# Optimization experiments

Measured on AMD Instinct MI355X. Metric: run time of the kernel, lower is better.

The kernel has to match this reference:

```python
import jax, jax.numpy as jnp
import numpy as np

N_HEAD = 16

def setup_inputs() -> dict:
    key = jax.random.key(0)
    k1, k2, k3 = jax.random.split(key, 3)
    B, T, D = 2, 2048, 1024
    x = jax.random.normal(k1, (B, T, D), dtype=jnp.float32)
    sigma_qkv = float(np.sqrt(2.0 / (D + 3 * D)))
    sigma_out = float(np.sqrt(2.0 / (D + D)))
    W_qkv = jax.random.truncated_normal(k2, -3.0, 3.0, (3 * D, D), dtype=jnp.float32) * sigma_qkv
    W_out = jax.random.truncated_normal(k3, -3.0, 3.0, (D, D), dtype=jnp.float32) * sigma_out
    return {"x": x, "W_qkv": W_qkv, "W_out": W_out}


def reference(x, W_qkv, W_out):
    B, T, C = x.shape
    H = N_HEAD
    hd = C // H
    qkv = x @ W_qkv.T  # (B,T,3C)
    q, k, v = jnp.split(qkv, 3, axis=-1)
    # (B,T,C) -> (B,H,T,hd)
    q = q.reshape(B, T, H, hd).transpose(0, 2, 1, 3)
    k = k.reshape(B, T, H, hd).transpose(0, 2, 1, 3)
    v = v.reshape(B, T, H, hd).transpose(0, 2, 1, 3)
    scale = 1.0 / jnp.sqrt(jnp.asarray(hd, dtype=x.dtype))
    score = jnp.einsum('bhqd,bhkd->bhqk', q, k) * scale  # (B,H,T,T)
    causal = jnp.tril(jnp.ones((T, T), dtype=bool))
    score = jnp.where(causal, score, -jnp.inf)
    attn = jax.nn.softmax(score, axis=-1)
    out = jnp.einsum('bhqk,bhkd->bhqd', attn, v)  # (B,H,T,hd)
    out = out.transpose(0, 2, 1, 3).reshape(B, T, C)
    return out @ W_out.T
```

## Files before the change

### kernel.cpp

```cpp
#include <hip/hip_runtime.h>
#include <hip/hip_bf16.h>
#include <cstdint>

typedef unsigned short u16;
typedef __attribute__((ext_vector_type(8))) short bf16x8;
typedef __attribute__((ext_vector_type(4))) float f32x4;

#define T_SEQ 2048
#define NHEAD 16
#define HDIM  64
#define NB    2

__device__ __forceinline__ float bf2f(uint32_t h) { return __uint_as_float(h << 16); }
__device__ __forceinline__ u16 f2bf(float f) {
    uint32_t u = __float_as_uint(f);
    u += 0x7fffu + ((u >> 16) & 1u);
    return (u16)(u >> 16);
}

__device__ __forceinline__ void gl_lds16(const u16* g, u16* s) {
    __builtin_amdgcn_global_load_lds(
        (const __attribute__((address_space(1))) unsigned int*)g,
        (__attribute__((address_space(3))) unsigned int*)s, 16, 0, 0);
}

__global__ void detect_dtype(const uint32_t* __restrict__ x, int* __restrict__ flag) {
    __shared__ int red[4];
    int c = 0;
#pragma unroll
    for (int j = 0; j < 4; j++) {
        uint32_t v = x[threadIdx.x * 4 + j];
        uint32_t lo = v & 0xffffu;
        uint32_t e = (lo >> 7) & 0xffu;
        if (lo != 0u && e >= 110u && e <= 135u) c++;
    }
#pragma unroll
    for (int off = 32; off; off >>= 1) c += __shfl_down(c, off);
    if ((threadIdx.x & 63) == 0) red[threadIdx.x >> 6] = c;
    __syncthreads();
    if (threadIdx.x == 0)
        *flag = (red[0] + red[1] + red[2] + red[3] > 614) ? 1 : 0;
}

__global__ __launch_bounds__(256) void to_bf16(
    const void* __restrict__ src, u16* __restrict__ dst, int n4,
    const int* __restrict__ flag)
{
    int i = blockIdx.x * 256 + threadIdx.x;
    const int stride = gridDim.x * 256;
    if (*flag != 0) {
        const uint2* s = (const uint2*)src;
        uint2* d = (uint2*)dst;
        for (; i < n4; i += stride) d[i] = s[i];
    } else {
        const float4* s = (const float4*)src;
        for (; i < n4; i += stride) {
            float4 v = s[i];
            ushort4 o = { f2bf(v.x), f2bf(v.y), f2bf(v.z), f2bf(v.w) };
            *(ushort4*)(dst + (size_t)i * 4) = o;
        }
    }
}

template<int BM, int MODE>
__global__ __launch_bounds__(256, 3) void gemm_bt_mfma(
    const u16* __restrict__ A, const u16* __restrict__ B,
    int N, int K,
    u16* __restrict__ qo, u16* __restrict__ ko, u16* __restrict__ vt,
    u16* __restrict__ outb16, float* __restrict__ outf32,
    const int* __restrict__ flag)
{
    constexpr int WM = BM / 2;
    constexpr int MI = WM / 16;
    constexpr int IA = BM / 32;
    constexpr int ST = 2 * BM * 64 * 2;
    constexpr int E16 = 4 * WM * 72 * 2;
    constexpr int EF = (MODE == 1) ? 4 * WM * (WM + 4) * 4 : 0;
    constexpr int SB = (ST > E16 ? ST : E16) > EF ? (ST > E16 ? ST : E16) : EF;
    __shared__ u16 smem[SB / 2];
    u16* As = smem;
    u16* Bs = smem + BM * 64;
    const int tid = threadIdx.x;
    const int bm = blockIdx.y * BM, bn = blockIdx.x * BM;
    const int w = tid >> 6, lane = tid & 63;
    const int wm = (w >> 1) * WM, wn = (w & 1) * WM;
    const int n16 = lane & 15, quad = lane >> 4;
    const int l8 = lane >> 3, c8 = lane & 7;

    f32x4 acc[MI][MI];
#pragma unroll
    for (int mi = 0; mi < MI; mi++)
#pragma unroll
        for (int ni = 0; ni < MI; ni++) acc[mi][ni] = (f32x4){0.f, 0.f, 0.f, 0.f};

    const int KT = K >> 6;
    for (int kt = 0; kt < KT; kt++) {
        const int k0 = kt << 6;
#pragma unroll
        for (int i = 0; i < IA; i++) {
            int rowblk = (i * 4 + w) * 8;
            int row = rowblk + l8;
            int gcol = (c8 ^ l8) * 8;
            gl_lds16(A + (size_t)(bm + row) * K + k0 + gcol, As + rowblk * 64);
            gl_lds16(B + (size_t)(bn + row) * K + k0 + gcol, Bs + rowblk * 64);
        }
        __syncthreads();
#pragma unroll
        for (int ks = 0; ks < 2; ks++) {
            bf16x8 af[MI], bfr[MI];
#pragma unroll
            for (int mi = 0; mi < MI; mi++) {
                int row = wm + mi * 16 + n16;
                af[mi] = *(const bf16x8*)(As + row * 64 + (((ks * 4 + quad) ^ (n16 & 7)) * 8));
            }
#pragma unroll
            for (int ni = 0; ni < MI; ni++) {
                int row = wn + ni * 16 + n16;
                bfr[ni] = *(const bf16x8*)(Bs + row * 64 + (((ks * 4 + quad) ^ (n16 & 7)) * 8));
            }
#pragma unroll
            for (int mi = 0; mi < MI; mi++)
#pragma unroll
                for (int ni = 0; ni < MI; ni++)
                    acc[mi][ni] = __builtin_amdgcn_mfma_f32_16x16x32_bf16(
                        af[mi], bfr[ni], acc[mi][ni], 0, 0, 0);
        }
        __syncthreads();
    }

    if constexpr (MODE == 0) {
        u16* ep = smem + w * (WM * 72);
        const int which = (bn + wn) >> 10;
        const int hq = ((bn + wn) & 1023) >> 6;
        const int bb = (bm + wm) >> 11;
        const int tb = (bm + wm) & (T_SEQ - 1);
        if (which == 2) {
#pragma unroll
            for (int mi = 0; mi < MI; mi++)
#pragma unroll
                for (int ni = 0; ni < MI; ni++)
#pragma unroll
                    for (int r = 0; r < 4; r++)
                        ep[(ni * 16 + n16) * 72 + mi * 16 + quad * 4 + r] = f2bf(acc[mi][ni][r]);
            asm volatile("s_waitcnt lgkmcnt(0)" ::: "memory");
            u16* dst = vt + ((size_t)(bb * NHEAD + hq) * HDIM) * T_SEQ + tb;
#pragma unroll
            for (int it = 0; it < 8; it++) {
                int row = it * 8 + l8, col = c8 * 8;
                bf16x8 v = *(const bf16x8*)(ep + row * 72 + col);
                *(bf16x8*)(dst + (size_t)row * T_SEQ + col) = v;
            }
        } else {
            const float sc = which ? 1.f : 0.125f;
#pragma unroll
            for (int mi = 0; mi < MI; mi++)
#pragma unroll
                for (int ni = 0; ni < MI; ni++)
#pragma unroll
                    for (int r = 0; r < 4; r++)
                        ep[(mi * 16 + quad * 4 + r) * 72 + ni * 16 + n16] = f2bf(acc[mi][ni][r] * sc);
            asm volatile("s_waitcnt lgkmcnt(0)" ::: "memory");
            u16* dst = (which ? ko : qo) + ((size_t)(bb * NHEAD + hq) * T_SEQ + tb) * HDIM;
#pragma unroll
            for (int it = 0; it < 8; it++) {
                int row = it * 8 + l8, col = c8 * 8;
                bf16x8 v = *(const bf16x8*)(ep + row * 72 + col);
                *(bf16x8*)(dst + (size_t)row * HDIM + col) = v;
            }
        }
    } else {
        if (*flag == 0) {
            float* epf = (float*)smem + w * (WM * (WM + 4));
#pragma unroll
            for (int mi = 0; mi < MI; mi++)
#pragma unroll
                for (int ni = 0; ni < MI; ni++)
#pragma unroll
                    for (int r = 0; r < 4; r++)
                        epf[(mi * 16 + quad * 4 + r) * (WM + 4) + ni * 16 + n16] = acc[mi][ni][r];
            asm volatile("s_waitcnt lgkmcnt(0)" ::: "memory");
            constexpr int LPR = WM / 4;
            constexpr int RPI = 64 / LPR;
#pragma unroll
            for (int it = 0; it < WM / RPI; it++) {
                int row = it * RPI + lane / LPR, col = (lane % LPR) * 4;
                float4 v = *(const float4*)(epf + row * (WM + 4) + col);
                *(float4*)(outf32 + (size_t)(bm + wm + row) * N + bn + wn + col) = v;
            }
        } else {
            u16* ep = smem + w * (WM * 72);
#pragma unroll
            for (int mi = 0; mi < MI; mi++)
#pragma unroll
                for (int ni = 0; ni < MI; ni++)
#pragma unroll
                    for (int r = 0; r < 4; r++)
                        ep[(mi * 16 + quad * 4 + r) * 72 + ni * 16 + n16] = f2bf(acc[mi][ni][r]);
            asm volatile("s_waitcnt lgkmcnt(0)" ::: "memory");
            constexpr int LPR = WM / 8;
            constexpr int RPI = 64 / LPR;
#pragma unroll
            for (int it = 0; it < WM / RPI; it++) {
                int row = it * RPI + lane / LPR, col = (lane % LPR) * 8;
                bf16x8 v = *(const bf16x8*)(ep + row * 72 + col);
                *(bf16x8*)(outb16 + (size_t)(bm + wm + row) * N + bn + wn + col) = v;
            }
        }
    }
}

__global__ __launch_bounds__(512, 4) void attn_mfma(
    const u16* __restrict__ qb, const u16* __restrict__ kb,
    const u16* __restrict__ vt, u16* __restrict__ ob)
{
    __shared__ u16 Ks[64 * 64];
    __shared__ u16 Vs[64 * 64];
    __shared__ u16 Plds[8][16][72];
    const int bidx = blockIdx.x;
    const int c = bidx & 255;
    const int rr = bidx >> 8;
    const int bh = c & 31;
    const int jm = c >> 5;
    const int t = rr ? (15 - jm) : jm;
    const int w = threadIdx.x >> 6, lane = threadIdx.x & 63;
    const int n16 = lane & 15, quad = lane >> 4;
    const int l8 = lane >> 3, c8 = lane & 7;
    const size_t baseK = (size_t)bh * T_SEQ * HDIM;
    const size_t baseV = (size_t)bh * HDIM * T_SEQ;
    const int b = bh >> 4, head = bh & 15;

    bf16x8 ones;
#pragma unroll
    for (int e = 0; e < 8; e++) ones[e] = (short)0x3F80;

    auto stage = [&](int kt) {
        int row = w * 8 + l8;
        int gc = (c8 ^ l8) * 8;
        gl_lds16(kb + baseK + (size_t)(kt * 64 + row) * HDIM + gc, Ks + (w * 8) * 64);
        gl_lds16(vt + baseV + (size_t)row * T_SEQ + (size_t)kt * 64 + gc, Vs + (w * 8) * 64);
    };

    const int qrow = t * 128 + w * 16;
    bf16x8 qf[2];
#pragma unroll
    for (int ks = 0; ks < 2; ks++)
        qf[ks] = *(const bf16x8*)(qb + baseK + (size_t)(qrow + n16) * HDIM + ks * 32 + quad * 8);

    f32x4 accO[4];
#pragma unroll
    for (int st = 0; st < 4; st++) accO[st] = (f32x4){0.f, 0.f, 0.f, 0.f};
    f32x4 accL = (f32x4){0.f, 0.f, 0.f, 0.f};

    const int ktmax = 2 * t + 1;
    const int kend  = 2 * t + (w >> 2);

    stage(0);
    for (int kt = 0; kt <= ktmax; kt++) {
        __syncthreads();

        const bool act = (kt <= kend);
        bf16x8 kf[2][4], vf[2][4];
        if (act) {
#pragma unroll
            for (int st = 0; st < 4; st++)
#pragma unroll
                for (int ks = 0; ks < 2; ks++) {
                    int off = (st * 16 + n16) * 64 + (((ks * 4 + quad) ^ (n16 & 7)) * 8);
                    kf[ks][st] = *(const bf16x8*)(Ks + off);
                    vf[ks][st] = *(const bf16x8*)(Vs + off);
                }
        }
        __syncthreads();

        if (kt < ktmax) stage(kt + 1);

        if (act) {
            f32x4 S[4];
#pragma unroll
            for (int st = 0; st < 4; st++) S[st] = (f32x4){0.f, 0.f, 0.f, 0.f};
#pragma unroll
            for (int st = 0; st < 4; st++)
#pragma unroll
                for (int ks = 0; ks < 2; ks++)
                    S[st] = __builtin_amdgcn_mfma_f32_16x16x32_bf16(qf[ks], kf[ks][st], S[st], 0, 0, 0);
            if (kt == kend) {
                int qloc = (w & 3) * 16 + quad * 4;
#pragma unroll
                for (int st = 0; st < 4; st++) {
                    int kloc = st * 16 + n16;
#pragma unroll
                    for (int r = 0; r < 4; r++)
                        if (kloc > qloc + r) S[st][r] = -INFINITY;
                }
            }
#pragma unroll
            for (int st = 0; st < 4; st++)
#pragma unroll
                for (int r = 0; r < 4; r++) {
                    float pv = exp2f(__builtin_fmaf(S[st][r], 1.44269504f, -14.4269504f));
                    Plds[w][quad * 4 + r][st * 16 + n16] = (u16)(__float_as_uint(pv) >> 16);
                }
            asm volatile("s_waitcnt lgkmcnt(0)" ::: "memory");
            bf16x8 pf[2];
#pragma unroll
            for (int ks = 0; ks < 2; ks++)
                pf[ks] = *(const bf16x8*)(&Plds[w][n16][ks * 32 + quad * 8]);
#pragma unroll
            for (int st = 0; st < 4; st++)
#pragma unroll
                for (int ks = 0; ks < 2; ks++)
                    accO[st] = __builtin_amdgcn_mfma_f32_16x16x32_bf16(pf[ks], vf[ks][st], accO[st], 0, 0, 0);
#pragma unroll
            for (int ks = 0; ks < 2; ks++)
                accL = __builtin_amdgcn_mfma_f32_16x16x32_bf16(pf[ks], ones, accL, 0, 0, 0);
        }
    }

#pragma unroll
    for (int r = 0; r < 4; r++) {
        float inv = 1.f / accL[r];
#pragma unroll
        for (int st = 0; st < 4; st++)
            Plds[w][quad * 4 + r][st * 16 + n16] = f2bf(accO[st][r] * inv);
    }
    asm volatile("s_waitcnt lgkmcnt(0)" ::: "memory");
    u16* dst = ob + ((size_t)(b * T_SEQ + qrow)) * 1024 + head * HDIM;
#pragma unroll
    for (int it = 0; it < 2; it++) {
        int row = it * 8 + l8, col = c8 * 8;
        bf16x8 v = *(const bf16x8*)(&Plds[w][row][col]);
        *(bf16x8*)(dst + (size_t)row * 1024 + col) = v;
    }
}

extern "C" void kernel_launch(void* const* d_in, const int* in_sizes, int n_in,
                              void* d_out, int out_size, void* d_ws, size_t ws_size,
                              hipStream_t stream) {
    const void* x    = d_in[0];
    const void* Wqkv = d_in[1];
    const void* Wout = d_in[2];

    const int Mtok = NB * T_SEQ;
    const size_t n_x    = (size_t)Mtok * 1024;
    const size_t n_wqkv = (size_t)3072 * 1024;
    const size_t n_wout = (size_t)1024 * 1024;
    const size_t qkv_elems = (size_t)NB * NHEAD * T_SEQ * HDIM;

    u16* xb    = (u16*)d_ws;
    u16* wqkvb = xb + n_x;
    u16* woutb = wqkvb + n_wqkv;
    u16* qb    = woutb + n_wout;
    u16* kb    = qb + qkv_elems;
    u16* vt    = kb + qkv_elems;
    u16* obuf  = vt + qkv_elems;
    int* flag  = (int*)(obuf + qkv_elems);

    detect_dtype<<<1, 256, 0, stream>>>((const uint32_t*)x, flag);

    to_bf16<<<1024, 256, 0, stream>>>(x,    xb,    (int)(n_x / 4),    flag);
    to_bf16<<<1024, 256, 0, stream>>>(Wqkv, wqkvb, (int)(n_wqkv / 4), flag);
    to_bf16<<<512,  256, 0, stream>>>(Wout, woutb, (int)(n_wout / 4), flag);

    gemm_bt_mfma<128, 0><<<dim3(3072 / 128, Mtok / 128), 256, 0, stream>>>(
        xb, wqkvb, 3072, 1024, qb, kb, vt, nullptr, nullptr, flag);

    attn_mfma<<<dim3(NB * NHEAD * (T_SEQ / 128)), 512, 0, stream>>>(qb, kb, vt, obuf);

    gemm_bt_mfma<64, 1><<<dim3(1024 / 64, Mtok / 64), 256, 0, stream>>>(
        obuf, woutb, 1024, 1024, nullptr, nullptr, nullptr,
        (u16*)d_out, (float*)d_out, flag);
}
```

Baseline: 171.1 us.

## Split attention KV loop across two warp groups with LDS combine

Doubles the attention block to 1024 threads. Two groups of 8 warps each handle alternating 64-key tiles for the same 128 query rows, then combine partial outputs and row sums through shared memory before normalising. Block scheduling also changes to longest-first ordering, replacing the previous paired balancing. This halves the serial KV-loop length per block, in exchange for an extra combine step, larger blocks and more register and LDS pressure per CU. The softmax uses a fixed max offset, so partial sums add directly.

After: 177.6 us. 1.04x slower.

```diff
diff --git a/kernel.cpp b/kernel.cpp
--- a/kernel.cpp
+++ b/kernel.cpp
@@ -209,38 +209,40 @@
     }
 }
 
-__global__ __launch_bounds__(512, 4) void attn_mfma(
+__global__ __launch_bounds__(1024, 4) void attn_mfma(
     const u16* __restrict__ qb, const u16* __restrict__ kb,
     const u16* __restrict__ vt, u16* __restrict__ ob)
 {
-    __shared__ u16 Ks[64 * 64];
-    __shared__ u16 Vs[64 * 64];
-    __shared__ u16 Plds[8][16][72];
+    __shared__ u16 KV[4 * 64 * 64];
+    __shared__ u16 Plds[16][16][72];
     const int bidx = blockIdx.x;
-    const int c = bidx & 255;
-    const int rr = bidx >> 8;
-    const int bh = c & 31;
-    const int jm = c >> 5;
-    const int t = rr ? (15 - jm) : jm;
+    const int bh = bidx & 31;
+    const int t  = 15 - (bidx >> 5);
     const int w = threadIdx.x >> 6, lane = threadIdx.x & 63;
+    const int g = w >> 3;
+    const int wq = w & 7;
     const int n16 = lane & 15, quad = lane >> 4;
     const int l8 = lane >> 3, c8 = lane & 7;
     const size_t baseK = (size_t)bh * T_SEQ * HDIM;
     const size_t baseV = (size_t)bh * HDIM * T_SEQ;
     const int b = bh >> 4, head = bh & 15;
 
+    u16* Ksg = KV + g * (2 * 64 * 64);
+    u16* Vsg = KV + g * (2 * 64 * 64) + 64 * 64;
+
     bf16x8 ones;
 #pragma unroll
     for (int e = 0; e < 8; e++) ones[e] = (short)0x3F80;
 
-    auto stage = [&](int kt) {
-        int row = w * 8 + l8;
+    auto stage = [&](int i) {
+        int kt = 2 * i + g;
+        int row = wq * 8 + l8;
         int gc = (c8 ^ l8) * 8;
-        gl_lds16(kb + baseK + (size_t)(kt * 64 + row) * HDIM + gc, Ks + (w * 8) * 64);
-        gl_lds16(vt + baseV + (size_t)row * T_SEQ + (size_t)kt * 64 + gc, Vs + (w * 8) * 64);
+        gl_lds16(kb + baseK + (size_t)(kt * 64 + row) * HDIM + gc, Ksg + (wq * 8) * 64);
+        gl_lds16(vt + baseV + (size_t)row * T_SEQ + (size_t)kt * 64 + gc, Vsg + (wq * 8) * 64);
     };
 
-    const int qrow = t * 128 + w * 16;
+    const int qrow = t * 128 + wq * 16;
     bf16x8 qf[2];
 #pragma unroll
     for (int ks = 0; ks < 2; ks++)
@@ -251,29 +253,24 @@
     for (int st = 0; st < 4; st++) accO[st] = (f32x4){0.f, 0.f, 0.f, 0.f};
     f32x4 accL = (f32x4){0.f, 0.f, 0.f, 0.f};
 
-    const int ktmax = 2 * t + 1;
-    const int kend  = 2 * t + (w >> 2);
-
     stage(0);
-    for (int kt = 0; kt <= ktmax; kt++) {
+    for (int i = 0; i <= t; i++) {
         __syncthreads();
 
-        const bool act = (kt <= kend);
         bf16x8 kf[2][4], vf[2][4];
-        if (act) {
-#pragma unroll
-            for (int st = 0; st < 4; st++)
-#pragma unroll
-                for (int ks = 0; ks < 2; ks++) {
-                    int off = (st * 16 + n16) * 64 + (((ks * 4 + quad) ^ (n16 & 7)) * 8);
-                    kf[ks][st] = *(const bf16x8*)(Ks + off);
-                    vf[ks][st] = *(const bf16x8*)(Vs + off);
-                }
-        }
+#pragma unroll
+        for (int st = 0; st < 4; st++)
+#pragma unroll
+            for (int ks = 0; ks < 2; ks++) {
+                int off = (st * 16 + n16) * 64 + (((ks * 4 + quad) ^ (n16 & 7)) * 8);
+                kf[ks][st] = *(const bf16x8*)(Ksg + off);
+                vf[ks][st] = *(const bf16x8*)(Vsg + off);
+            }
         __syncthreads();
 
-        if (kt < ktmax) stage(kt + 1);
-
+        if (i < t) stage(i + 1);
+
+        const bool act = (i < t) | (g == 0) | (wq >= 4);
         if (act) {
             f32x4 S[4];
 #pragma unroll
@@ -283,11 +280,12 @@
 #pragma unroll
                 for (int ks = 0; ks < 2; ks++)
                     S[st] = __builtin_amdgcn_mfma_f32_16x16x32_bf16(qf[ks], kf[ks][st], S[st], 0, 0, 0);
-            if (kt == kend) {
-                int qloc = (w & 3) * 16 + quad * 4;
+            if (i == t) {
+                const int kbase = g * 64;
+                int qloc = wq * 16 + quad * 4;
 #pragma unroll
                 for (int st = 0; st < 4; st++) {
-                    int kloc = st * 16 + n16;
+                    int kloc = kbase + st * 16 + n16;
 #pragma unroll
                     for (int r = 0; r < 4; r++)
                         if (kloc > qloc + r) S[st][r] = -INFINITY;
@@ -316,20 +314,42 @@
         }
     }
 
-#pragma unroll
-    for (int r = 0; r < 4; r++) {
-        float inv = 1.f / accL[r];
+    float* cmbO = (float*)KV;
+    float* cmbL = (float*)&Plds[8][0][0];
+    if (g == 1) {
 #pragma unroll
         for (int st = 0; st < 4; st++)
-            Plds[w][quad * 4 + r][st * 16 + n16] = f2bf(accO[st][r] * inv);
-    }
-    asm volatile("s_waitcnt lgkmcnt(0)" ::: "memory");
-    u16* dst = ob + ((size_t)(b * T_SEQ + qrow)) * 1024 + head * HDIM;
-#pragma unroll
-    for (int it = 0; it < 2; it++) {
-        int row = it * 8 + l8, col = c8 * 8;
-        bf16x8 v = *(const bf16x8*)(&Plds[w][row][col]);
-        *(bf16x8*)(dst + (size_t)row * 1024 + col) = v;
+#pragma unroll
+            for (int r = 0; r < 4; r++)
+                cmbO[wq * 1024 + (quad * 4 + r) * 64 + st * 16 + n16] = accO[st][r];
+        if (n16 == 0)
+#pragma unroll
+            for (int r = 0; r < 4; r++)
+                cmbL[wq * 16 + quad * 4 + r] = accL[r];
+    }
+    __syncthreads();
+    if (g == 0) {
+#pragma unroll
+        for (int st = 0; st < 4; st++)
+#pragma unroll
+            for (int r = 0; r < 4; r++)
+                accO[st][r] += cmbO[wq * 1024 + (quad * 4 + r) * 64 + st * 16 + n16];
+#pragma unroll
+        for (int r = 0; r < 4; r++) {
+            float l2 = cmbL[wq * 16 + quad * 4 + r];
+            float inv = 1.f / (accL[r] + l2);
+#pragma unroll
+            for (int st = 0; st < 4; st++)
+                Plds[w][quad * 4 + r][st * 16 + n16] = f2bf(accO[st][r] * inv);
+        }
+        asm volatile("s_waitcnt lgkmcnt(0)" ::: "memory");
+        u16* dst = ob + ((size_t)(b * T_SEQ + qrow)) * 1024 + head * HDIM;
+#pragma unroll
+        for (int it = 0; it < 2; it++) {
+            int row = it * 8 + l8, col = c8 * 8;
+            bf16x8 v = *(const bf16x8*)(&Plds[w][row][col]);
+            *(bf16x8*)(dst + (size_t)row * 1024 + col) = v;
+        }
     }
 }
 
@@ -364,7 +384,7 @@
     gemm_bt_mfma<128, 0><<<dim3(3072 / 128, Mtok / 128), 256, 0, stream>>>(
         xb, wqkvb, 3072, 1024, qb, kb, vt, nullptr, nullptr, flag);
 
-    attn_mfma<<<dim3(NB * NHEAD * (T_SEQ / 128)), 512, 0, stream>>>(qb, kb, vt, obuf);
+    attn_mfma<<<dim3(NB * NHEAD * (T_SEQ / 128)), 1024, 0, stream>>>(qb, kb, vt, obuf);
 
     gemm_bt_mfma<64, 1><<<dim3(1024 / 64, Mtok / 64), 256, 0, stream>>>(
         obuf, woutb, 1024, 1024, nullptr, nullptr, nullptr,
```

## Halve attention block threads, each wave handles two 16-row query subtiles

Applied to the files above, without the earlier changes.

The attention kernel now runs with 256 threads (4 waves) instead of 512, and each wave processes 32 query rows as two 16-row subtiles. K and V fragments loaded from LDS are reused across both subtiles, which halves LDS read traffic per query row. Each wave also stages twice as many rows. The change adds register pressure (two accumulator sets) and gives fewer waves per block to hide latency, and the launch bounds are lowered accordingly.

Result: slower. 180.9 us (+5.8%).

```diff
diff --git a/kernel.cpp b/kernel.cpp
--- a/kernel.cpp
+++ b/kernel.cpp
@@ -209,13 +209,13 @@
     }
 }
 
-__global__ __launch_bounds__(512, 4) void attn_mfma(
+__global__ __launch_bounds__(256, 3) void attn_mfma(
     const u16* __restrict__ qb, const u16* __restrict__ kb,
     const u16* __restrict__ vt, u16* __restrict__ ob)
 {
     __shared__ u16 Ks[64 * 64];
     __shared__ u16 Vs[64 * 64];
-    __shared__ u16 Plds[8][16][72];
+    __shared__ u16 Plds[4][2][16][72];
     const int bidx = blockIdx.x;
     const int c = bidx & 255;
     const int rr = bidx >> 8;
@@ -234,25 +234,36 @@
     for (int e = 0; e < 8; e++) ones[e] = (short)0x3F80;
 
     auto stage = [&](int kt) {
-        int row = w * 8 + l8;
-        int gc = (c8 ^ l8) * 8;
-        gl_lds16(kb + baseK + (size_t)(kt * 64 + row) * HDIM + gc, Ks + (w * 8) * 64);
-        gl_lds16(vt + baseV + (size_t)row * T_SEQ + (size_t)kt * 64 + gc, Vs + (w * 8) * 64);
+#pragma unroll
+        for (int i = 0; i < 2; i++) {
+            int rowblk = w * 16 + i * 8;
+            int row = rowblk + l8;
+            int gc = (c8 ^ l8) * 8;
+            gl_lds16(kb + baseK + (size_t)(kt * 64 + row) * HDIM + gc, Ks + rowblk * 64);
+            gl_lds16(vt + baseV + (size_t)row * T_SEQ + (size_t)kt * 64 + gc, Vs + rowblk * 64);
+        }
     };
 
-    const int qrow = t * 128 + w * 16;
-    bf16x8 qf[2];
-#pragma unroll
-    for (int ks = 0; ks < 2; ks++)
-        qf[ks] = *(const bf16x8*)(qb + baseK + (size_t)(qrow + n16) * HDIM + ks * 32 + quad * 8);
-
-    f32x4 accO[4];
-#pragma unroll
-    for (int st = 0; st < 4; st++) accO[st] = (f32x4){0.f, 0.f, 0.f, 0.f};
-    f32x4 accL = (f32x4){0.f, 0.f, 0.f, 0.f};
+    const int qrow = t * 128 + w * 32;
+    bf16x8 qf[2][2];
+#pragma unroll
+    for (int s = 0; s < 2; s++)
+#pragma unroll
+        for (int ks = 0; ks < 2; ks++)
+            qf[s][ks] = *(const bf16x8*)(qb + baseK +
+                (size_t)(qrow + s * 16 + n16) * HDIM + ks * 32 + quad * 8);
+
+    f32x4 accO[2][4];
+#pragma unroll
+    for (int s = 0; s < 2; s++)
+#pragma unroll
+        for (int st = 0; st < 4; st++) accO[s][st] = (f32x4){0.f, 0.f, 0.f, 0.f};
+    f32x4 accL[2];
+    accL[0] = (f32x4){0.f, 0.f, 0.f, 0.f};
+    accL[1] = (f32x4){0.f, 0.f, 0.f, 0.f};
 
     const int ktmax = 2 * t + 1;
-    const int kend  = 2 * t + (w >> 2);
+    const int kend  = 2 * t + (w >> 1);
 
     stage(0);
     for (int kt = 0; kt <= ktmax; kt++) {
@@ -275,61 +286,70 @@
         if (kt < ktmax) stage(kt + 1);
 
         if (act) {
-            f32x4 S[4];
-#pragma unroll
-            for (int st = 0; st < 4; st++) S[st] = (f32x4){0.f, 0.f, 0.f, 0.f};
+#pragma unroll
+            for (int s = 0; s < 2; s++) {
+                f32x4 S[4];
+#pragma unroll
+                for (int st = 0; st < 4; st++) S[st] = (f32x4){0.f, 0.f, 0.f, 0.f};
+#pragma unroll
+                for (int st = 0; st < 4; st++)
+#pragma unroll
+                    for (int ks = 0; ks < 2; ks++)
+                        S[st] = __builtin_amdgcn_mfma_f32_16x16x32_bf16(qf[s][ks], kf[ks][st], S[st], 0, 0, 0);
+                if (kt == kend) {
+                    int qloc = w * 32 + s * 16 + quad * 4 - (w >> 1) * 64;
+#pragma unroll
+                    for (int st = 0; st < 4; st++) {
+                        int kloc = st * 16 + n16;
+#pragma unroll
+                        for (int r = 0; r < 4; r++)
+                            if (kloc > qloc + r) S[st][r] = -INFINITY;
+                    }
+                }
+#pragma unroll
+                for (int st = 0; st < 4; st++)
+#pragma unroll
+                    for (int r = 0; r < 4; r++) {
+                        float pv = exp2f(__builtin_fmaf(S[st][r], 1.44269504f, -14.4269504f));
+                        Plds[w][s][quad * 4 + r][st * 16 + n16] = (u16)(__float_as_uint(pv) >> 16);
+                    }
+                asm volatile("s_waitcnt lgkmcnt(0)" ::: "memory");
+                bf16x8 pf[2];
+#pragma unroll
+                for (int ks = 0; ks < 2; ks++)
+                    pf[ks] = *(const bf16x8*)(&Plds[w][s][n16][ks * 32 + quad * 8]);
+#pragma unroll
+                for (int st = 0; st < 4; st++)
+#pragma unroll
+                    for (int ks = 0; ks < 2; ks++)
+                        accO[s][st] = __builtin_amdgcn_mfma_f32_16x16x32_bf16(pf[ks], vf[ks][st], accO[s][st], 0, 0, 0);
+#pragma unroll
+                for (int ks = 0; ks < 2; ks++)
+                    accL[s] = __builtin_amdgcn_mfma_f32_16x16x32_bf16(pf[ks], ones, accL[s], 0, 0, 0);
+            }
+        }
+    }
+
+#pragma unroll
+    for (int s = 0; s < 2; s++) {
+#pragma unroll
+        for (int r = 0; r < 4; r++) {
+            float inv = 1.f / accL[s][r];
 #pragma unroll
             for (int st = 0; st < 4; st++)
-#pragma unroll
-                for (int ks = 0; ks < 2; ks++)
-                    S[st] = __builtin_amdgcn_mfma_f32_16x16x32_bf16(qf[ks], kf[ks][st], S[st], 0, 0, 0);
-            if (kt == kend) {
-                int qloc = (w & 3) * 16 + quad * 4;
-#pragma unroll
-                for (int st = 0; st < 4; st++) {
-                    int kloc = st * 16 + n16;
-#pragma unroll
-                    for (int r = 0; r < 4; r++)
-                        if (kloc > qloc + r) S[st][r] = -INFINITY;
-                }
-            }
-#pragma unroll
-            for (int st = 0; st < 4; st++)
-#pragma unroll
-                for (int r = 0; r < 4; r++) {
-                    float pv = exp2f(__builtin_fmaf(S[st][r], 1.44269504f, -14.4269504f));
-                    Plds[w][quad * 4 + r][st * 16 + n16] = (u16)(__float_as_uint(pv) >> 16);
-                }
-            asm volatile("s_waitcnt lgkmcnt(0)" ::: "memory");
-            bf16x8 pf[2];
-#pragma unroll
-            for (int ks = 0; ks < 2; ks++)
-                pf[ks] = *(const bf16x8*)(&Plds[w][n16][ks * 32 + quad * 8]);
-#pragma unroll
-            for (int st = 0; st < 4; st++)
-#pragma unroll
-                for (int ks = 0; ks < 2; ks++)
-                    accO[st] = __builtin_amdgcn_mfma_f32_16x16x32_bf16(pf[ks], vf[ks][st], accO[st], 0, 0, 0);
-#pragma unroll
-            for (int ks = 0; ks < 2; ks++)
-                accL = __builtin_amdgcn_mfma_f32_16x16x32_bf16(pf[ks], ones, accL, 0, 0, 0);
-        }
-    }
-
-#pragma unroll
-    for (int r = 0; r < 4; r++) {
-        float inv = 1.f / accL[r];
-#pragma unroll
-        for (int st = 0; st < 4; st++)
-            Plds[w][quad * 4 + r][st * 16 + n16] = f2bf(accO[st][r] * inv);
+                Plds[w][s][quad * 4 + r][st * 16 + n16] = f2bf(accO[s][st][r] * inv);
+        }
     }
     asm volatile("s_waitcnt lgkmcnt(0)" ::: "memory");
-    u16* dst = ob + ((size_t)(b * T_SEQ + qrow)) * 1024 + head * HDIM;
-#pragma unroll
-    for (int it = 0; it < 2; it++) {
-        int row = it * 8 + l8, col = c8 * 8;
-        bf16x8 v = *(const bf16x8*)(&Plds[w][row][col]);
-        *(bf16x8*)(dst + (size_t)row * 1024 + col) = v;
+#pragma unroll
+    for (int s = 0; s < 2; s++) {
+        u16* dst = ob + ((size_t)(b * T_SEQ + qrow + s * 16)) * 1024 + head * HDIM;
+#pragma unroll
+        for (int it = 0; it < 2; it++) {
+            int row = it * 8 + l8, col = c8 * 8;
+            bf16x8 v = *(const bf16x8*)(&Plds[w][s][row][col]);
+            *(bf16x8*)(dst + (size_t)row * 1024 + col) = v;
+        }
     }
 }
 
@@ -364,7 +384,7 @@
     gemm_bt_mfma<128, 0><<<dim3(3072 / 128, Mtok / 128), 256, 0, stream>>>(
         xb, wqkvb, 3072, 1024, qb, kb, vt, nullptr, nullptr, flag);
 
-    attn_mfma<<<dim3(NB * NHEAD * (T_SEQ / 128)), 512, 0, stream>>>(qb, kb, vt, obuf);
+    attn_mfma<<<dim3(NB * NHEAD * (T_SEQ / 128)), 256, 0, stream>>>(qb, kb, vt, obuf);
 
     gemm_bt_mfma<64, 1><<<dim3(1024 / 64, Mtok / 64), 256, 0, stream>>>(
         obuf, woutb, 1024, 1024, nullptr, nullptr, nullptr,
```
